# Optimization experiments

Measured on AMD Instinct MI355X. Metric: run time of the kernel, lower is better.

Reference implementation:

```python
import jax, jax.numpy as jnp
import numpy as np

Q_DIM, V_DIM, HID = 768, 512, 512


def setup_inputs() -> dict:
    key = jax.random.key(0)
    kV, kQ, kwq, kbq, kwv, kbv = jax.random.split(key, 6)
    B, Nv, Nq = 64, 1024, 512
    V = jax.random.normal(kV, (B, Nv, V_DIM), dtype=jnp.float32)
    Q = jax.random.normal(kQ, (B, Nq, Q_DIM), dtype=jnp.float32)
    # torch Linear params: weight [out, in], bias [out]
    Wq_w = jax.random.normal(kwq, (HID, Q_DIM), dtype=jnp.float32) / np.sqrt(Q_DIM)
    Wq_b = jax.random.normal(kbq, (HID,), dtype=jnp.float32) * 0.01
    Wv_w = jax.random.normal(kwv, (HID, V_DIM), dtype=jnp.float32) / np.sqrt(V_DIM)
    Wv_b = jax.random.normal(kbv, (HID,), dtype=jnp.float32) * 0.01
    return {"V": V, "Q": Q, "Wq_w": Wq_w, "Wq_b": Wq_b, "Wv_w": Wv_w, "Wv_b": Wv_b}


def reference(V, Q, Wq_w, Wq_b, Wv_w, Wv_b):
    # Q_proj: [B, Nq, HID]; V_proj: [B, Nv, HID]
    Q_proj = jnp.einsum('bqd,hd->bqh', Q, Wq_w) + Wq_b
    V_proj = jnp.einsum('bvd,hd->bvh', V, Wv_w) + Wv_b
    # H: [B, Nq, Nv]
    H = jnp.tanh(jnp.einsum('bqh,bvh->bqv', Q_proj, V_proj))
    A_v = jax.nn.softmax(H, axis=2)              # over Nv
    V_tilde = jnp.einsum('bqv,bvd->bqd', A_v, V)  # [B, Nq, V_DIM]
    A_q = jax.nn.softmax(H, axis=1)              # softmax(H^T, dim=2) == softmax over Nq
    Q_tilde = jnp.einsum('bqv,bqd->bvd', A_q, Q)  # [B, Nv, Q_DIM]
    v_hat = V_tilde.sum(axis=1)                   # [B, V_DIM]
    q_hat = Q_tilde.sum(axis=1)                   # [B, Q_DIM]
    return (v_hat, q_hat)
```

## Files before the change

### kernel.cpp

```cpp
#include <hip/hip_runtime.h>
#include <hip/hip_bf16.h>
#include <math.h>

#define B_SZ 64
#define NQ   512
#define NV   1024
#define QD   768
#define VD   512
#define HIDD 512

typedef __bf16 bf16x8 __attribute__((ext_vector_type(8)));
typedef __bf16 bf16x4 __attribute__((ext_vector_type(4)));
typedef float  floatx4 __attribute__((ext_vector_type(4)));

__device__ __forceinline__ void g2lds16(const __bf16* g, __bf16* l) {
    __builtin_amdgcn_global_load_lds((const __attribute__((address_space(1))) void*)g,
                                     (__attribute__((address_space(3))) void*)l,
                                     16, 0, 0);
}

__device__ __forceinline__ float exptanh(float s) {
    float t = __expf(2.0f * s);
    float r = __builtin_amdgcn_rcpf(t + 1.0f);
    return __expf(1.0f - 2.0f * r);
}

__global__ __launch_bounds__(256) void cvt_k(const float* __restrict__ s,
                                             __bf16* __restrict__ d, int n4) {
    int i = blockIdx.x * 256 + threadIdx.x;
    if (i < n4) {
        float4 f = *(const float4*)(s + (size_t)i * 4);
        bf16x4 o;
        o[0] = (__bf16)f.x; o[1] = (__bf16)f.y; o[2] = (__bf16)f.z; o[3] = (__bf16)f.w;
        *(bf16x4*)(d + (size_t)i * 4) = o;
    }
}

template<int K>
__global__ __launch_bounds__(256, 2) void gemm_proj(
    const float* __restrict__ A, const __bf16* __restrict__ Wb,
    const float* __restrict__ bias, __bf16* __restrict__ Cout)
{
    __shared__ __bf16 As[64 * 32];
    __shared__ __bf16 Bs[512 * 32];
    const int t = threadIdx.x, lane = t & 63, wave = t >> 6;
    const int fr = lane & 15, quad = lane >> 4, fo = quad * 8;
    const int tile_m = blockIdx.x * 64;
    const int wn = wave * 128;

    const int arow = t >> 2, akc = (t & 3) * 8;
    const float* ap = A + (size_t)(tile_m + arow) * K + akc;

    const __bf16* wsrc = Wb + (size_t)(wave * 128 + (lane >> 2)) * K + (lane & 3) * 8;
    __bf16* bbase = &Bs[wave * 128 * 32];

    floatx4 acc[4][8] = {};
    for (int k0 = 0; k0 < K; k0 += 32) {
        #pragma unroll
        for (int c = 0; c < 8; c++)
            g2lds16(wsrc + (size_t)(c * 16) * K + k0, bbase + c * 512);
        float4 f0 = *(const float4*)(ap + k0);
        float4 f1 = *(const float4*)(ap + k0 + 4);
        bf16x8 p;
        p[0] = (__bf16)f0.x; p[1] = (__bf16)f0.y; p[2] = (__bf16)f0.z; p[3] = (__bf16)f0.w;
        p[4] = (__bf16)f1.x; p[5] = (__bf16)f1.y; p[6] = (__bf16)f1.z; p[7] = (__bf16)f1.w;
        *(bf16x8*)&As[arow * 32 + akc] = p;
        __syncthreads();
        bf16x8 af[4];
        #pragma unroll
        for (int i = 0; i < 4; i++)
            af[i] = *(const bf16x8*)&As[(16 * i + fr) * 32 + fo];
        #pragma unroll
        for (int j = 0; j < 8; j++) {
            bf16x8 bg = *(const bf16x8*)&Bs[(wn + 16 * j + fr) * 32 + fo];
            #pragma unroll
            for (int i = 0; i < 4; i++)
                acc[i][j] = __builtin_amdgcn_mfma_f32_16x16x32_bf16(af[i], bg, acc[i][j], 0, 0, 0);
        }
        __syncthreads();
    }
    #pragma unroll
    for (int j = 0; j < 8; j++) {
        const int col = wn + 16 * j + fr;
        const float bv = bias[col];
        #pragma unroll
        for (int i = 0; i < 4; i++)
            #pragma unroll
            for (int r = 0; r < 4; r++) {
                const int row = tile_m + 16 * i + quad * 4 + r;
                Cout[(size_t)row * HIDD + col] = (__bf16)(acc[i][j][r] + bv);
            }
    }
}

__global__ __launch_bounds__(256) void gemm_h(
    const __bf16* __restrict__ Qp, const __bf16* __restrict__ Vp,
    __bf16* __restrict__ Eg, float* __restrict__ R, float* __restrict__ Csum)
{
    __shared__ __bf16 As[128 * 32];
    __shared__ __bf16 Bs[128 * 32];
    const int b      = blockIdx.z;
    const int tile_q = blockIdx.y * 128;
    const int tile_v = blockIdx.x * 128;
    const int t = threadIdx.x, lane = t & 63, wave = t >> 6;
    const int wm = (wave >> 1) * 64, wn = (wave & 1) * 64;
    const int fr = lane & 15, quad = lane >> 4, fo = quad * 8;

    const int grow = wave * 32 + (lane >> 2);
    const int gk   = (lane & 3) * 8;
    const __bf16* Aq = Qp + ((size_t)b * NQ + tile_q + grow) * HIDD + gk;
    const __bf16* Bv = Vp + ((size_t)b * NV + tile_v + grow) * HIDD + gk;
    __bf16* asw = &As[wave * 1024];
    __bf16* bsw = &Bs[wave * 1024];

    floatx4 acc[4][4] = {};
    for (int k0 = 0; k0 < HIDD; k0 += 32) {
        g2lds16(Aq + k0, asw);
        g2lds16(Aq + (size_t)16 * HIDD + k0, asw + 512);
        g2lds16(Bv + k0, bsw);
        g2lds16(Bv + (size_t)16 * HIDD + k0, bsw + 512);
        __syncthreads();
        bf16x8 af[4], bg[4];
        #pragma unroll
        for (int i = 0; i < 4; i++)
            af[i] = *(const bf16x8*)&As[(wm + 16 * i + fr) * 32 + fo];
        #pragma unroll
        for (int j = 0; j < 4; j++)
            bg[j] = *(const bf16x8*)&Bs[(wn + 16 * j + fr) * 32 + fo];
        #pragma unroll
        for (int i = 0; i < 4; i++)
            #pragma unroll
            for (int j = 0; j < 4; j++)
                acc[i][j] = __builtin_amdgcn_mfma_f32_16x16x32_bf16(af[i], bg[j], acc[i][j], 0, 0, 0);
        __syncthreads();
    }

    #pragma unroll
    for (int i = 0; i < 4; i++)
        #pragma unroll
        for (int j = 0; j < 4; j++)
            #pragma unroll
            for (int r = 0; r < 4; r++)
                acc[i][j][r] = exptanh(acc[i][j][r]);

    #pragma unroll
    for (int i = 0; i < 4; i++)
        #pragma unroll
        for (int r = 0; r < 4; r++) {
            const size_t rowbase =
                ((size_t)b * NQ + tile_q + wm + 16 * i + quad * 4 + r) * NV + tile_v;
            #pragma unroll
            for (int j = 0; j < 4; j++)
                Eg[rowbase + wn + 16 * j + fr] = (__bf16)acc[i][j][r];
        }

    float rs[4][4];
    #pragma unroll
    for (int i = 0; i < 4; i++)
        #pragma unroll
        for (int r = 0; r < 4; r++) {
            float s = acc[i][0][r] + acc[i][1][r] + acc[i][2][r] + acc[i][3][r];
            s += __shfl_xor(s, 1); s += __shfl_xor(s, 2);
            s += __shfl_xor(s, 4); s += __shfl_xor(s, 8);
            rs[i][r] = s;
        }
    if (fr == 0) {
        #pragma unroll
        for (int i = 0; i < 4; i++)
            #pragma unroll
            for (int r = 0; r < 4; r++)
                atomicAdd(&R[b * NQ + tile_q + wm + 16 * i + quad * 4 + r], rs[i][r]);
    }
    float cs[4];
    #pragma unroll
    for (int j = 0; j < 4; j++) {
        float s = 0.f;
        #pragma unroll
        for (int i = 0; i < 4; i++)
            #pragma unroll
            for (int r = 0; r < 4; r++)
                s += acc[i][j][r];
        s += __shfl_xor(s, 16); s += __shfl_xor(s, 32);
        cs[j] = s;
    }
    if (quad == 0) {
        #pragma unroll
        for (int j = 0; j < 4; j++)
            atomicAdd(&Csum[b * NV + tile_v + wn + 16 * j + fr], cs[j]);
    }
}

__global__ __launch_bounds__(256) void marg_k(
    const __bf16* __restrict__ E, const float* __restrict__ R,
    const float* __restrict__ C, float* __restrict__ sv,
    float* __restrict__ sq)
{
    const int b  = blockIdx.y;
    const int q0 = blockIdx.x * 64;
    const int t = threadIdx.x, lane = t & 63, wave = t >> 6;
    const float* Cb = C + b * NV;
    float ci[2][8];
    float svp[2][8] = {};
    #pragma unroll
    for (int c = 0; c < 2; c++) {
        float4 c0 = *(const float4*)&Cb[c * 512 + lane * 8];
        float4 c1 = *(const float4*)&Cb[c * 512 + lane * 8 + 4];
        ci[c][0] = 1.0f / c0.x; ci[c][1] = 1.0f / c0.y;
        ci[c][2] = 1.0f / c0.z; ci[c][3] = 1.0f / c0.w;
        ci[c][4] = 1.0f / c1.x; ci[c][5] = 1.0f / c1.y;
        ci[c][6] = 1.0f / c1.z; ci[c][7] = 1.0f / c1.w;
    }
    const float* Rb = R + b * NQ + q0;
    for (int rr = 0; rr < 16; rr++) {
        const int q = wave * 16 + rr;
        const __bf16* Erow = E + ((size_t)b * NQ + q0 + q) * NV;
        const float ri = 1.0f / Rb[q];
        float p = 0.f;
        #pragma unroll
        for (int c = 0; c < 2; c++) {
            bf16x8 ev = *(const bf16x8*)&Erow[c * 512 + lane * 8];
            #pragma unroll
            for (int k = 0; k < 8; k++) {
                float e = (float)ev[k];
                svp[c][k] += e * ri;
                p += e * ci[c][k];
            }
        }
        p += __shfl_xor(p, 1);  p += __shfl_xor(p, 2);  p += __shfl_xor(p, 4);
        p += __shfl_xor(p, 8);  p += __shfl_xor(p, 16); p += __shfl_xor(p, 32);
        if (lane == 0) sq[b * NQ + q0 + q] = p;
    }
    #pragma unroll
    for (int c = 0; c < 2; c++)
        #pragma unroll
        for (int k = 0; k < 8; k++)
            atomicAdd(&sv[b * NV + c * 512 + lane * 8 + k], svp[c][k]);
}

__global__ __launch_bounds__(256) void vhat_k(const float* __restrict__ sv,
                                              const float* __restrict__ V,
                                              float* __restrict__ out) {
    const int b  = blockIdx.y;
    const int v0 = blockIdx.z * 256;
    const int d  = blockIdx.x * 256 + threadIdx.x;
    const float* Vb  = V + ((size_t)b * NV + v0) * VD + d;
    const float* svb = sv + b * NV + v0;
    float acc = 0.f;
    #pragma unroll 8
    for (int v = 0; v < 256; v++) acc += svb[v] * Vb[(size_t)v * VD];
    atomicAdd(&out[b * VD + d], acc);
}

__global__ __launch_bounds__(256) void qhat_k(const float* __restrict__ sq,
                                              const float* __restrict__ Q,
                                              float* __restrict__ out) {
    const int b  = blockIdx.y;
    const int q0 = blockIdx.z * 256;
    const int d  = blockIdx.x * 256 + threadIdx.x;
    const float* Qb  = Q + ((size_t)b * NQ + q0) * QD + d;
    const float* sqb = sq + b * NQ + q0;
    float acc = 0.f;
    #pragma unroll 8
    for (int q = 0; q < 256; q++) acc += sqb[q] * Qb[(size_t)q * QD];
    atomicAdd(&out[b * QD + d], acc);
}

extern "C" void kernel_launch(void* const* d_in, const int* in_sizes, int n_in,
                              void* d_out, int out_size, void* d_ws, size_t ws_size,
                              hipStream_t stream) {
    const float* V    = (const float*)d_in[0];
    const float* Q    = (const float*)d_in[1];
    const float* Wq_w = (const float*)d_in[2];
    const float* Wq_b = (const float*)d_in[3];
    const float* Wv_w = (const float*)d_in[4];
    const float* Wv_b = (const float*)d_in[5];
    float* out = (float*)d_out;

    const size_t nQp = (size_t)B_SZ * NQ * HIDD;
    const size_t nVp = (size_t)B_SZ * NV * HIDD;
    const size_t nE  = (size_t)B_SZ * NQ * NV;
    const size_t nWq = (size_t)HIDD * QD;
    const size_t nWv = (size_t)HIDD * VD;
    __bf16* Qp = (__bf16*)d_ws;
    __bf16* Vp = Qp + nQp;
    __bf16* E  = Vp + nVp;
    float* R   = (float*)(E + nE);
    float* C   = R + (size_t)B_SZ * NQ;
    float* sv  = C + (size_t)B_SZ * NV;
    float* sq  = sv + (size_t)B_SZ * NV;
    __bf16* Wq = (__bf16*)(sq + (size_t)B_SZ * NQ);
    __bf16* Wv = Wq + nWq;
    size_t need = (nQp + nVp + nE + nWq + nWv) * 2 +
                  ((size_t)B_SZ * (NQ + NV) * 2) * 4;
    if (ws_size < need) return;

    hipMemsetAsync(R, 0, (size_t)B_SZ * (NQ + NV) * 2 * sizeof(float), stream);
    hipMemsetAsync(d_out, 0, (size_t)out_size * sizeof(float), stream);

    cvt_k<<<(int)(nWq / 1024), 256, 0, stream>>>(Wq_w, Wq, (int)(nWq / 4));
    cvt_k<<<(int)(nWv / 1024), 256, 0, stream>>>(Wv_w, Wv, (int)(nWv / 4));

    gemm_proj<QD><<<(B_SZ * NQ) / 64, 256, 0, stream>>>(Q, Wq, Wq_b, Qp);
    gemm_proj<VD><<<(B_SZ * NV) / 64, 256, 0, stream>>>(V, Wv, Wv_b, Vp);

    gemm_h<<<dim3(NV / 128, NQ / 128, B_SZ), 256, 0, stream>>>(Qp, Vp, E, R, C);

    marg_k<<<dim3(NQ / 64, B_SZ), 256, 0, stream>>>(E, R, C, sv, sq);

    vhat_k<<<dim3(VD / 256, B_SZ, NV / 256), 256, 0, stream>>>(sv, V, out);
    qhat_k<<<dim3(QD / 256, B_SZ, NQ / 256), 256, 0, stream>>>(sq, Q, out + (size_t)B_SZ * VD);
}
```

Baseline: 532.7 us.

## Double-buffer and swizzle GEMMs, merge launches, retile H GEMM and reductions

```diff
diff --git a/kernel.cpp b/kernel.cpp
--- a/kernel.cpp
+++ b/kernel.cpp
@@ -25,120 +25,165 @@
     return __expf(1.0f - 2.0f * r);
 }
 
-__global__ __launch_bounds__(256) void cvt_k(const float* __restrict__ s,
-                                             __bf16* __restrict__ d, int n4) {
+__global__ __launch_bounds__(256) void cvt2_k(const float* __restrict__ s0,
+                                              const float* __restrict__ s1,
+                                              __bf16* __restrict__ d,
+                                              int n4a, int n4tot) {
     int i = blockIdx.x * 256 + threadIdx.x;
-    if (i < n4) {
-        float4 f = *(const float4*)(s + (size_t)i * 4);
-        bf16x4 o;
-        o[0] = (__bf16)f.x; o[1] = (__bf16)f.y; o[2] = (__bf16)f.z; o[3] = (__bf16)f.w;
-        *(bf16x4*)(d + (size_t)i * 4) = o;
-    }
-}
-
-template<int K>
-__global__ __launch_bounds__(256, 2) void gemm_proj(
-    const float* __restrict__ A, const __bf16* __restrict__ Wb,
-    const float* __restrict__ bias, __bf16* __restrict__ Cout)
+    if (i >= n4tot) return;
+    const float* s = (i < n4a) ? (s0 + (size_t)i * 4) : (s1 + (size_t)(i - n4a) * 4);
+    float4 f = *(const float4*)s;
+    bf16x4 o;
+    o[0] = (__bf16)f.x; o[1] = (__bf16)f.y; o[2] = (__bf16)f.z; o[3] = (__bf16)f.w;
+    *(bf16x4*)(d + (size_t)i * 4) = o;
+}
+
+__global__ __launch_bounds__(256, 2) void proj_k(
+    const float* __restrict__ Qin, const float* __restrict__ Vin,
+    const __bf16* __restrict__ Wqb, const __bf16* __restrict__ Wvb,
+    const float* __restrict__ bq, const float* __restrict__ bv,
+    __bf16* __restrict__ Qp, __bf16* __restrict__ Vp)
 {
-    __shared__ __bf16 As[64 * 32];
-    __shared__ __bf16 Bs[512 * 32];
+    __shared__ __bf16 As[2][64 * 32];
+    __shared__ __bf16 Bs[2][512 * 32];
+    const int nqblk = (B_SZ * NQ) / 64;
+    const float* A; const __bf16* W; const float* bias; __bf16* Cout; int K, mblk;
+    if ((int)blockIdx.x < nqblk) {
+        A = Qin; W = Wqb; bias = bq; Cout = Qp; K = QD; mblk = blockIdx.x;
+    } else {
+        A = Vin; W = Wvb; bias = bv; Cout = Vp; K = VD; mblk = blockIdx.x - nqblk;
+    }
+
     const int t = threadIdx.x, lane = t & 63, wave = t >> 6;
-    const int fr = lane & 15, quad = lane >> 4, fo = quad * 8;
-    const int tile_m = blockIdx.x * 64;
+    const int fr = lane & 15, quad = lane >> 4;
+    const int fo   = (quad ^ ((fr >> 1) & 3)) * 8;
+    const int gksw = ((lane & 3) ^ ((lane >> 3) & 3)) * 8;
+    const int tile_m = mblk * 64;
     const int wn = wave * 128;
 
-    const int arow = t >> 2, akc = (t & 3) * 8;
-    const float* ap = A + (size_t)(tile_m + arow) * K + akc;
-
-    const __bf16* wsrc = Wb + (size_t)(wave * 128 + (lane >> 2)) * K + (lane & 3) * 8;
-    __bf16* bbase = &Bs[wave * 128 * 32];
+    const __bf16* wsrc = W + (size_t)(wave * 16 + (lane >> 2)) * K + gksw;
+    const int arow = t >> 2, aslot = t & 3;
+    const float* ap = A + (size_t)(tile_m + arow) * K + aslot * 8;
+    const int awoff = arow * 32 + ((aslot ^ ((arow >> 1) & 3)) * 8);
 
     floatx4 acc[4][8] = {};
-    for (int k0 = 0; k0 < K; k0 += 32) {
+
+    auto stage_w = [&](int p, int k0) {
         #pragma unroll
         for (int c = 0; c < 8; c++)
-            g2lds16(wsrc + (size_t)(c * 16) * K + k0, bbase + c * 512);
+            g2lds16(wsrc + (size_t)(c * 64) * K + k0, &Bs[p][(c * 64 + wave * 16) * 32]);
+    };
+    auto cvt_a = [&](int p, float4 f0, float4 f1) {
+        bf16x8 pk;
+        pk[0] = (__bf16)f0.x; pk[1] = (__bf16)f0.y; pk[2] = (__bf16)f0.z; pk[3] = (__bf16)f0.w;
+        pk[4] = (__bf16)f1.x; pk[5] = (__bf16)f1.y; pk[6] = (__bf16)f1.z; pk[7] = (__bf16)f1.w;
+        *(bf16x8*)&As[p][awoff] = pk;
+    };
+    auto compute = [&](int p) {
+        bf16x8 af[4];
+        #pragma unroll
+        for (int i = 0; i < 4; i++)
+            af[i] = *(const bf16x8*)&As[p][(16 * i + fr) * 32 + fo];
+        #pragma unroll
+        for (int j = 0; j < 8; j++) {
+            bf16x8 bg = *(const bf16x8*)&Bs[p][(wn + 16 * j + fr) * 32 + fo];
+            #pragma unroll
+            for (int i = 0; i < 4; i++)
+                acc[i][j] = __builtin_amdgcn_mfma_f32_16x16x32_bf16(af[i], bg, acc[i][j], 0, 0, 0);
+        }
+    };
+
+    {
+        float4 f0 = *(const float4*)(ap);
+        float4 f1 = *(const float4*)(ap + 4);
+        stage_w(0, 0);
+        cvt_a(0, f0, f1);
+    }
+    __syncthreads();
+    int cur = 0;
+    for (int k0 = 32; k0 < K; k0 += 32) {
         float4 f0 = *(const float4*)(ap + k0);
         float4 f1 = *(const float4*)(ap + k0 + 4);
-        bf16x8 p;
-        p[0] = (__bf16)f0.x; p[1] = (__bf16)f0.y; p[2] = (__bf16)f0.z; p[3] = (__bf16)f0.w;
-        p[4] = (__bf16)f1.x; p[5] = (__bf16)f1.y; p[6] = (__bf16)f1.z; p[7] = (__bf16)f1.w;
-        *(bf16x8*)&As[arow * 32 + akc] = p;
+        const int nxt = cur ^ 1;
+        stage_w(nxt, k0);
+        compute(cur);
+        cvt_a(nxt, f0, f1);
         __syncthreads();
-        bf16x8 af[4];
-        #pragma unroll
-        for (int i = 0; i < 4; i++)
-            af[i] = *(const bf16x8*)&As[(16 * i + fr) * 32 + fo];
-        #pragma unroll
-        for (int j = 0; j < 8; j++) {
-            bf16x8 bg = *(const bf16x8*)&Bs[(wn + 16 * j + fr) * 32 + fo];
-            #pragma unroll
-            for (int i = 0; i < 4; i++)
-                acc[i][j] = __builtin_amdgcn_mfma_f32_16x16x32_bf16(af[i], bg, acc[i][j], 0, 0, 0);
-        }
-        __syncthreads();
-    }
+        cur = nxt;
+    }
+    compute(cur);
+
     #pragma unroll
     for (int j = 0; j < 8; j++) {
         const int col = wn + 16 * j + fr;
-        const float bv = bias[col];
+        const float bvv = bias[col];
         #pragma unroll
         for (int i = 0; i < 4; i++)
             #pragma unroll
             for (int r = 0; r < 4; r++) {
                 const int row = tile_m + 16 * i + quad * 4 + r;
-                Cout[(size_t)row * HIDD + col] = (__bf16)(acc[i][j][r] + bv);
+                Cout[(size_t)row * HIDD + col] = (__bf16)(acc[i][j][r] + bvv);
             }
     }
 }
 
-__global__ __launch_bounds__(256) void gemm_h(
+__global__ __launch_bounds__(256, 2) void gemm_h(
     const __bf16* __restrict__ Qp, const __bf16* __restrict__ Vp,
     __bf16* __restrict__ Eg, float* __restrict__ R, float* __restrict__ Csum)
 {
-    __shared__ __bf16 As[128 * 32];
-    __shared__ __bf16 Bs[128 * 32];
+    __shared__ __bf16 As[2][128 * 32];
+    __shared__ __bf16 Bs[2][256 * 32];
     const int b      = blockIdx.z;
     const int tile_q = blockIdx.y * 128;
-    const int tile_v = blockIdx.x * 128;
+    const int tile_v = blockIdx.x * 256;
     const int t = threadIdx.x, lane = t & 63, wave = t >> 6;
-    const int wm = (wave >> 1) * 64, wn = (wave & 1) * 64;
-    const int fr = lane & 15, quad = lane >> 4, fo = quad * 8;
-
-    const int grow = wave * 32 + (lane >> 2);
-    const int gk   = (lane & 3) * 8;
-    const __bf16* Aq = Qp + ((size_t)b * NQ + tile_q + grow) * HIDD + gk;
-    const __bf16* Bv = Vp + ((size_t)b * NV + tile_v + grow) * HIDD + gk;
-    __bf16* asw = &As[wave * 1024];
-    __bf16* bsw = &Bs[wave * 1024];
-
-    floatx4 acc[4][4] = {};
-    for (int k0 = 0; k0 < HIDD; k0 += 32) {
-        g2lds16(Aq + k0, asw);
-        g2lds16(Aq + (size_t)16 * HIDD + k0, asw + 512);
-        g2lds16(Bv + k0, bsw);
-        g2lds16(Bv + (size_t)16 * HIDD + k0, bsw + 512);
+    const int fr = lane & 15, quad = lane >> 4;
+    const int fo   = (quad ^ ((fr >> 1) & 3)) * 8;
+    const int gksw = ((lane & 3) ^ ((lane >> 3) & 3)) * 8;
+    const int wm = (wave >> 1) * 64, wn = (wave & 1) * 128;
+
+    const __bf16* Aq = Qp + ((size_t)b * NQ + tile_q + wave * 16 + (lane >> 2)) * HIDD + gksw;
+    const __bf16* Bv = Vp + ((size_t)b * NV + tile_v + wave * 16 + (lane >> 2)) * HIDD + gksw;
+
+    auto stage = [&](int p, int k0) {
+        #pragma unroll
+        for (int c = 0; c < 2; c++)
+            g2lds16(Aq + (size_t)(c * 64) * HIDD + k0, &As[p][(c * 64 + wave * 16) * 32]);
+        #pragma unroll
+        for (int c = 0; c < 4; c++)
+            g2lds16(Bv + (size_t)(c * 64) * HIDD + k0, &Bs[p][(c * 64 + wave * 16) * 32]);
+    };
+
+    floatx4 acc[4][8] = {};
+    auto compute = [&](int p) {
+        bf16x8 af[4];
+        #pragma unroll
+        for (int i = 0; i < 4; i++)
+            af[i] = *(const bf16x8*)&As[p][(wm + 16 * i + fr) * 32 + fo];
+        #pragma unroll
+        for (int j = 0; j < 8; j++) {
+            bf16x8 bg = *(const bf16x8*)&Bs[p][(wn + 16 * j + fr) * 32 + fo];
+            #pragma unroll
+            for (int i = 0; i < 4; i++)
+                acc[i][j] = __builtin_amdgcn_mfma_f32_16x16x32_bf16(af[i], bg, acc[i][j], 0, 0, 0);
+        }
+    };
+
+    stage(0, 0);
+    __syncthreads();
+    int cur = 0;
+    for (int k0 = 32; k0 < HIDD; k0 += 32) {
+        stage(cur ^ 1, k0);
+        compute(cur);
         __syncthreads();
-        bf16x8 af[4], bg[4];
-        #pragma unroll
-        for (int i = 0; i < 4; i++)
-            af[i] = *(const bf16x8*)&As[(wm + 16 * i + fr) * 32 + fo];
-        #pragma unroll
-        for (int j = 0; j < 4; j++)
-            bg[j] = *(const bf16x8*)&Bs[(wn + 16 * j + fr) * 32 + fo];
-        #pragma unroll
-        for (int i = 0; i < 4; i++)
-            #pragma unroll
-            for (int j = 0; j < 4; j++)
-                acc[i][j] = __builtin_amdgcn_mfma_f32_16x16x32_bf16(af[i], bg[j], acc[i][j], 0, 0, 0);
-        __syncthreads();
-    }
+        cur ^= 1;
+    }
+    compute(cur);
 
     #pragma unroll
     for (int i = 0; i < 4; i++)
         #pragma unroll
-        for (int j = 0; j < 4; j++)
+        for (int j = 0; j < 8; j++)
             #pragma unroll
             for (int r = 0; r < 4; r++)
                 acc[i][j][r] = exptanh(acc[i][j][r]);
@@ -150,43 +195,32 @@
             const size_t rowbase =
                 ((size_t)b * NQ + tile_q + wm + 16 * i + quad * 4 + r) * NV + tile_v;
             #pragma unroll
-            for (int j = 0; j < 4; j++)
+            for (int j = 0; j < 8; j++)
                 Eg[rowbase + wn + 16 * j + fr] = (__bf16)acc[i][j][r];
         }
 
-    float rs[4][4];
     #pragma unroll
     for (int i = 0; i < 4; i++)
         #pragma unroll
         for (int r = 0; r < 4; r++) {
-            float s = acc[i][0][r] + acc[i][1][r] + acc[i][2][r] + acc[i][3][r];
+            float s = 0.f;
+            #pragma unroll
+            for (int j = 0; j < 8; j++) s += acc[i][j][r];
             s += __shfl_xor(s, 1); s += __shfl_xor(s, 2);
             s += __shfl_xor(s, 4); s += __shfl_xor(s, 8);
-            rs[i][r] = s;
-        }
-    if (fr == 0) {
+            if (fr == 0)
+                atomicAdd(&R[b * NQ + tile_q + wm + 16 * i + quad * 4 + r], s);
+        }
+    #pragma unroll
+    for (int j = 0; j < 8; j++) {
+        float s = 0.f;
         #pragma unroll
         for (int i = 0; i < 4; i++)
             #pragma unroll
-            for (int r = 0; r < 4; r++)
-                atomicAdd(&R[b * NQ + tile_q + wm + 16 * i + quad * 4 + r], rs[i][r]);
-    }
-    float cs[4];
-    #pragma unroll
-    for (int j = 0; j < 4; j++) {
-        float s = 0.f;
-        #pragma unroll
-        for (int i = 0; i < 4; i++)
-            #pragma unroll
-            for (int r = 0; r < 4; r++)
-                s += acc[i][j][r];
+            for (int r = 0; r < 4; r++) s += acc[i][j][r];
         s += __shfl_xor(s, 16); s += __shfl_xor(s, 32);
-        cs[j] = s;
-    }
-    if (quad == 0) {
-        #pragma unroll
-        for (int j = 0; j < 4; j++)
-            atomicAdd(&Csum[b * NV + tile_v + wn + 16 * j + fr], cs[j]);
+        if (quad == 0)
+            atomicAdd(&Csum[b * NV + tile_v + wn + 16 * j + fr], s);
     }
 }
 
@@ -196,7 +230,7 @@
     float* __restrict__ sq)
 {
     const int b  = blockIdx.y;
-    const int q0 = blockIdx.x * 64;
+    const int q0 = blockIdx.x * 16;
     const int t = threadIdx.x, lane = t & 63, wave = t >> 6;
     const float* Cb = C + b * NV;
     float ci[2][8];
@@ -211,8 +245,9 @@
         ci[c][6] = 1.0f / c1.z; ci[c][7] = 1.0f / c1.w;
     }
     const float* Rb = R + b * NQ + q0;
-    for (int rr = 0; rr < 16; rr++) {
-        const int q = wave * 16 + rr;
+    #pragma unroll
+    for (int rr = 0; rr < 4; rr++) {
+        const int q = wave * 4 + rr;
         const __bf16* Erow = E + ((size_t)b * NQ + q0 + q) * NV;
         const float ri = 1.0f / Rb[q];
         float p = 0.f;
@@ -241,28 +276,38 @@
                                               const float* __restrict__ V,
                                               float* __restrict__ out) {
     const int b  = blockIdx.y;
-    const int v0 = blockIdx.z * 256;
-    const int d  = blockIdx.x * 256 + threadIdx.x;
-    const float* Vb  = V + ((size_t)b * NV + v0) * VD + d;
+    const int v0 = blockIdx.x * 128;
+    const int t  = threadIdx.x;
+    const float* Vb  = V + ((size_t)b * NV + v0) * VD + t * 2;
     const float* svb = sv + b * NV + v0;
-    float acc = 0.f;
+    float ax = 0.f, ay = 0.f;
     #pragma unroll 8
-    for (int v = 0; v < 256; v++) acc += svb[v] * Vb[(size_t)v * VD];
-    atomicAdd(&out[b * VD + d], acc);
-}
-
-__global__ __launch_bounds__(256) void qhat_k(const float* __restrict__ sq,
+    for (int v = 0; v < 128; v++) {
+        const float s = svb[v];
+        const float2 val = *(const float2*)(Vb + (size_t)v * VD);
+        ax += s * val.x; ay += s * val.y;
+    }
+    atomicAdd(&out[b * VD + t * 2],     ax);
+    atomicAdd(&out[b * VD + t * 2 + 1], ay);
+}
+
+__global__ __launch_bounds__(384) void qhat_k(const float* __restrict__ sq,
                                               const float* __restrict__ Q,
                                               float* __restrict__ out) {
     const int b  = blockIdx.y;
-    const int q0 = blockIdx.z * 256;
-    const int d  = blockIdx.x * 256 + threadIdx.x;
-    const float* Qb  = Q + ((size_t)b * NQ + q0) * QD + d;
+    const int q0 = blockIdx.x * 64;
+    const int t  = threadIdx.x;
+    const float* Qb  = Q + ((size_t)b * NQ + q0) * QD + t * 2;
     const float* sqb = sq + b * NQ + q0;
-    float acc = 0.f;
+    float ax = 0.f, ay = 0.f;
     #pragma unroll 8
-    for (int q = 0; q < 256; q++) acc += sqb[q] * Qb[(size_t)q * QD];
-    atomicAdd(&out[b * QD + d], acc);
+    for (int q = 0; q < 64; q++) {
+        const float s = sqb[q];
+        const float2 val = *(const float2*)(Qb + (size_t)q * QD);
+        ax += s * val.x; ay += s * val.y;
+    }
+    atomicAdd(&out[b * QD + t * 2],     ax);
+    atomicAdd(&out[b * QD + t * 2 + 1], ay);
 }
 
 extern "C" void kernel_launch(void* const* d_in, const int* in_sizes, int n_in,
@@ -297,16 +342,16 @@
     hipMemsetAsync(R, 0, (size_t)B_SZ * (NQ + NV) * 2 * sizeof(float), stream);
     hipMemsetAsync(d_out, 0, (size_t)out_size * sizeof(float), stream);
 
-    cvt_k<<<(int)(nWq / 1024), 256, 0, stream>>>(Wq_w, Wq, (int)(nWq / 4));
-    cvt_k<<<(int)(nWv / 1024), 256, 0, stream>>>(Wv_w, Wv, (int)(nWv / 4));
-
-    gemm_proj<QD><<<(B_SZ * NQ) / 64, 256, 0, stream>>>(Q, Wq, Wq_b, Qp);
-    gemm_proj<VD><<<(B_SZ * NV) / 64, 256, 0, stream>>>(V, Wv, Wv_b, Vp);
-
-    gemm_h<<<dim3(NV / 128, NQ / 128, B_SZ), 256, 0, stream>>>(Qp, Vp, E, R, C);
-
-    marg_k<<<dim3(NQ / 64, B_SZ), 256, 0, stream>>>(E, R, C, sv, sq);
-
-    vhat_k<<<dim3(VD / 256, B_SZ, NV / 256), 256, 0, stream>>>(sv, V, out);
-    qhat_k<<<dim3(QD / 256, B_SZ, NQ / 256), 256, 0, stream>>>(sq, Q, out + (size_t)B_SZ * VD);
-}
+    cvt2_k<<<(int)((nWq + nWv) / 1024), 256, 0, stream>>>(
+        Wq_w, Wv_w, Wq, (int)(nWq / 4), (int)((nWq + nWv) / 4));
+
+    proj_k<<<(B_SZ * NQ) / 64 + (B_SZ * NV) / 64, 256, 0, stream>>>(
+        Q, V, Wq, Wv, Wq_b, Wv_b, Qp, Vp);
+
+    gemm_h<<<dim3(NV / 256, NQ / 128, B_SZ), 256, 0, stream>>>(Qp, Vp, E, R, C);
+
+    marg_k<<<dim3(NQ / 16, B_SZ), 256, 0, stream>>>(E, R, C, sv, sq);
+
+    vhat_k<<<dim3(NV / 128, B_SZ), 256, 0, stream>>>(sv, V, out);
+    qhat_k<<<dim3(NQ / 64, B_SZ), 384, 0, stream>>>(sq, Q, out + (size_t)B_SZ * VD);
+}
```

Measured after the change: 662.7 us. 24.4% more time.
